# Performance work log

Hardware: AMD Instinct MI355X
Metric: run time of the kernel (lower is better)

The kernel has to match this reference:

```python
import jax, jax.numpy as jnp
import numpy as np

N0, N1, N2 = 360448, 22528, 2048
E0, E1 = 337920, 20480
D = 256


def setup_inputs() -> dict:
    key = jax.random.key(0)
    ks = jax.random.split(key, 12)
    s = 1.0 / np.sqrt(D)
    return {
        "x": jax.random.normal(ks[0], (N0, D), dtype=jnp.float32),
        "src0": jax.random.randint(ks[1], (E0,), 0, N0, dtype=jnp.int32),
        "dst0": jax.random.randint(ks[2], (E0,), 0, N1, dtype=jnp.int32),
        "src1": jax.random.randint(ks[3], (E1,), 0, N1, dtype=jnp.int32),
        "dst1": jax.random.randint(ks[4], (E1,), 0, N2, dtype=jnp.int32),
        "Wl0": jax.random.normal(ks[5], (D, D), dtype=jnp.float32) * s,
        "bl0": jnp.zeros((D,), dtype=jnp.float32),
        "Wr0": jax.random.normal(ks[6], (D, D), dtype=jnp.float32) * s,
        "Wl1": jax.random.normal(ks[7], (D, D), dtype=jnp.float32) * s,
        "bl1": jnp.zeros((D,), dtype=jnp.float32),
        "Wr1": jax.random.normal(ks[8], (D, D), dtype=jnp.float32) * s,
    }


def _sage_conv(x_src, x_tgt, src, dst, n_tgt, Wl, bl, Wr):
    # mean aggregation of source neighbor features per target node
    summed = jax.ops.segment_sum(x_src[src], dst, num_segments=n_tgt)
    cnt = jax.ops.segment_sum(jnp.ones((src.shape[0],), x_src.dtype), dst,
                              num_segments=n_tgt)
    agg = summed / jnp.maximum(cnt, 1.0)[:, None]
    # PyG SAGEConv: lin_l(agg) + lin_r(x_target); lin_r has no bias
    return agg @ Wl.T + bl + x_tgt @ Wr.T


def reference(x, src0, dst0, src1, dst1, Wl0, bl0, Wr0, Wl1, bl1, Wr1):
    # layer 0: [N0, D] -> [N1, D]
    h = _sage_conv(x, x[:N1], src0, dst0, N1, Wl0, bl0, Wr0)
    h = jax.nn.relu(h)  # dropout is identity in eval mode
    # layer 1: [N1, D] -> [N2, D]
    out = _sage_conv(h, h[:N2], src1, dst1, N2, Wl1, bl1, Wr1)
    return out
```

## Files before the change

### kernel.cpp

```cpp
#include <hip/hip_runtime.h>
#include <hip/hip_bf16.h>

#define N1C 22528
#define N2C 2048

typedef __attribute__((ext_vector_type(8))) short bf16x8;
typedef __attribute__((ext_vector_type(4))) float f32x4;

__device__ __forceinline__ short f2bf(float f) {
    union { float f; unsigned u; } x; x.f = f;
    unsigned r = x.u + 0x7fff + ((x.u >> 16) & 1);
    return (short)(r >> 16);
}
__device__ __forceinline__ float bf2f(unsigned short u) {
    union { unsigned u; float f; } x; x.u = ((unsigned)u) << 16;
    return x.f;
}

__global__ void prep_kernel(const float* __restrict__ Wl0, const float* __restrict__ Wr0,
                            const float* __restrict__ Wl1, const float* __restrict__ Wr1,
                            short* __restrict__ Wcat0, short* __restrict__ Wcat1,
                            int* __restrict__ hist0, int* __restrict__ hist1) {
    const int stride = gridDim.x * blockDim.x;
    const int tid0 = blockIdx.x * blockDim.x + threadIdx.x;
    for (int i = tid0; i < 2 * 256 * 512; i += stride) {
        int layer = i >> 17;
        int r = i & ((1 << 17) - 1);
        int j = r >> 9, k = r & 511;
        const float* Wl = layer ? Wl1 : Wl0;
        const float* Wr = layer ? Wr1 : Wr0;
        float v = (k < 256) ? Wl[j * 256 + k] : Wr[j * 256 + (k - 256)];
        (layer ? Wcat1 : Wcat0)[r] = f2bf(v);
    }
    for (int i = tid0; i < N1C + N2C; i += stride) {
        if (i < N1C) hist0[i] = 0; else hist1[i - N1C] = 0;
    }
}

__global__ void hist_both_kernel(const int* __restrict__ dst0, int E0,
                                 const int* __restrict__ dst1, int E1,
                                 int* __restrict__ hist0, int* __restrict__ hist1) {
    const int stride = gridDim.x * blockDim.x;
    for (int i = blockIdx.x * blockDim.x + threadIdx.x; i < E0 + E1; i += stride) {
        if (i < E0) atomicAdd(&hist0[dst0[i]], 1);
        else        atomicAdd(&hist1[dst1[i - E0]], 1);
    }
}

__global__ __launch_bounds__(1024)
void scan_both_kernel(const int* __restrict__ hist0, int* __restrict__ rowptr0,
                      int* __restrict__ cursor0,
                      const int* __restrict__ hist1, int* __restrict__ rowptr1,
                      int* __restrict__ cursor1) {
    __shared__ int sums[1024];
    const int N = (blockIdx.x == 0) ? N1C : N2C;
    const int* hist   = (blockIdx.x == 0) ? hist0 : hist1;
    int* rowptr       = (blockIdx.x == 0) ? rowptr0 : rowptr1;
    int* cursor       = (blockIdx.x == 0) ? cursor0 : cursor1;
    const int tid = threadIdx.x;
    const int per = (N + 1023) >> 10;
    const int start = tid * per;
    const int end = min(start + per, N);
    int s = 0;
    for (int i = start; i < end; ++i) s += hist[i];
    sums[tid] = s;
    __syncthreads();
    for (int d = 1; d < 1024; d <<= 1) {
        int t = (tid >= d) ? sums[tid - d] : 0;
        __syncthreads();
        sums[tid] += t;
        __syncthreads();
    }
    int off = sums[tid] - s;
    for (int i = start; i < end; ++i) {
        rowptr[i] = off;
        cursor[i] = off;
        off += hist[i];
    }
    if (tid == 1023) rowptr[N] = off;
}

__global__ void fill_both_kernel(const int* __restrict__ src0, const int* __restrict__ dst0, int E0,
                                 const int* __restrict__ src1, const int* __restrict__ dst1, int E1,
                                 int* __restrict__ cursor0, int* __restrict__ eidx0,
                                 int* __restrict__ cursor1, int* __restrict__ eidx1) {
    const int stride = gridDim.x * blockDim.x;
    for (int i = blockIdx.x * blockDim.x + threadIdx.x; i < E0 + E1; i += stride) {
        if (i < E0) {
            int p = atomicAdd(&cursor0[dst0[i]], 1);
            eidx0[p] = src0[i];
        } else {
            int p = atomicAdd(&cursor1[dst1[i - E0]], 1);
            eidx1[p] = src1[i - E0];
        }
    }
}

template <bool SRC_F32>
__global__ __launch_bounds__(256)
void gather_mean_kernel(const void* __restrict__ Xv, const int* __restrict__ rowptr,
                        const int* __restrict__ eidx, short* __restrict__ Acat, int N) {
    const int wv = (blockIdx.x * 256 + threadIdx.x) >> 6;
    const int lane = threadIdx.x & 63;
    if (wv >= N) return;
    const int beg = rowptr[wv];
    const int end = rowptr[wv + 1];
    float a0 = 0.f, a1 = 0.f, a2 = 0.f, a3 = 0.f;
    int j = beg;
    if (SRC_F32) {
        const float* X = (const float*)Xv;
        for (; j + 1 < end; j += 2) {
            int s0 = eidx[j], s1 = eidx[j + 1];
            float4 v0 = *(const float4*)(X + (size_t)s0 * 256 + lane * 4);
            float4 v1 = *(const float4*)(X + (size_t)s1 * 256 + lane * 4);
            a0 += v0.x + v1.x; a1 += v0.y + v1.y;
            a2 += v0.z + v1.z; a3 += v0.w + v1.w;
        }
        if (j < end) {
            float4 v0 = *(const float4*)(X + (size_t)eidx[j] * 256 + lane * 4);
            a0 += v0.x; a1 += v0.y; a2 += v0.z; a3 += v0.w;
        }
    } else {
        const ushort* X = (const ushort*)Xv;
        for (; j + 1 < end; j += 2) {
            int s0 = eidx[j], s1 = eidx[j + 1];
            ushort4 v0 = *(const ushort4*)(X + (size_t)s0 * 256 + lane * 4);
            ushort4 v1 = *(const ushort4*)(X + (size_t)s1 * 256 + lane * 4);
            a0 += bf2f(v0.x) + bf2f(v1.x); a1 += bf2f(v0.y) + bf2f(v1.y);
            a2 += bf2f(v0.z) + bf2f(v1.z); a3 += bf2f(v0.w) + bf2f(v1.w);
        }
        if (j < end) {
            ushort4 v0 = *(const ushort4*)(X + (size_t)eidx[j] * 256 + lane * 4);
            a0 += bf2f(v0.x); a1 += bf2f(v0.y); a2 += bf2f(v0.z); a3 += bf2f(v0.w);
        }
    }
    const float sc = 1.0f / fmaxf((float)(end - beg), 1.0f);
    short4 o;
    o.x = f2bf(a0 * sc); o.y = f2bf(a1 * sc);
    o.z = f2bf(a2 * sc); o.w = f2bf(a3 * sc);
    *(short4*)(Acat + (size_t)wv * 512 + lane * 4) = o;
}

__global__ void xcast_kernel(const float* __restrict__ x, short* __restrict__ Acat0) {
    const int stride = gridDim.x * blockDim.x;
    const int total = N1C * 64;
    for (int u = blockIdx.x * blockDim.x + threadIdx.x; u < total; u += stride) {
        int row = u >> 6;
        int c = (u & 63) * 4;
        float4 v = *(const float4*)(x + (size_t)row * 256 + c);
        short4 o;
        o.x = f2bf(v.x); o.y = f2bf(v.y); o.z = f2bf(v.z); o.w = f2bf(v.w);
        *(short4*)(Acat0 + (size_t)row * 512 + 256 + c) = o;
    }
}

template <bool RELU, bool OUT_BF16>
__global__ __launch_bounds__(256)
void mfma_gemm_kernel(const short* __restrict__ A, const short* __restrict__ W,
                      const float* __restrict__ bias, void* __restrict__ out,
                      short* __restrict__ out2, int M) {
    const int tid = threadIdx.x;
    const int wave = tid >> 6;
    const int lane = tid & 63;
    const int r0 = blockIdx.x * 64 + wave * 16;
    const int j0 = blockIdx.y * 64;
    const int lrow = lane & 15;
    const int lk = (lane >> 4) * 8;

    const short* arow = A + (size_t)(r0 + lrow) * 512 + lk;
    const short* wbase = W + (size_t)(j0 + lrow) * 512 + lk;

    f32x4 acc[4] = {f32x4{0,0,0,0}, f32x4{0,0,0,0}, f32x4{0,0,0,0}, f32x4{0,0,0,0}};
#pragma unroll
    for (int ks = 0; ks < 16; ++ks) {
        bf16x8 a = *(const bf16x8*)(arow + ks * 32);
#pragma unroll
        for (int c = 0; c < 4; ++c) {
            bf16x8 b = *(const bf16x8*)(wbase + (size_t)c * 16 * 512 + ks * 32);
            acc[c] = __builtin_amdgcn_mfma_f32_16x16x32_bf16(a, b, acc[c], 0, 0, 0);
        }
    }

    const int orow = (lane >> 4) * 4;
#pragma unroll
    for (int c = 0; c < 4; ++c) {
        const int col = j0 + c * 16 + lrow;
        const float bv = bias[col];
#pragma unroll
        for (int i = 0; i < 4; ++i) {
            const int row = r0 + orow + i;
            float v = acc[c][i] + bv;
            if (RELU) v = fmaxf(v, 0.0f);
            if (OUT_BF16) {
                short hv = f2bf(v);
                ((short*)out)[(size_t)row * 256 + col] = hv;
                if (out2 != nullptr && row < N2C)
                    out2[(size_t)row * 512 + 256 + col] = hv;
            } else {
                ((float*)out)[(size_t)row * 256 + col] = v;
            }
        }
    }
}

extern "C" void kernel_launch(void* const* d_in, const int* in_sizes, int n_in,
                              void* d_out, int out_size, void* d_ws, size_t ws_size,
                              hipStream_t stream) {
    const float* x    = (const float*)d_in[0];
    const int*   src0 = (const int*)d_in[1];
    const int*   dst0 = (const int*)d_in[2];
    const int*   src1 = (const int*)d_in[3];
    const int*   dst1 = (const int*)d_in[4];
    const float* Wl0  = (const float*)d_in[5];
    const float* bl0  = (const float*)d_in[6];
    const float* Wr0  = (const float*)d_in[7];
    const float* Wl1  = (const float*)d_in[8];
    const float* bl1  = (const float*)d_in[9];
    const float* Wr1  = (const float*)d_in[10];

    const int E0 = in_sizes[1];
    const int E1 = in_sizes[3];

    char* p = (char*)d_ws;
    short* Acat0 = (short*)p;            p += (size_t)N1C * 512 * 2;
    short* h     = (short*)p;            p += (size_t)N1C * 256 * 2;
    short* Acat1 = (short*)p;            p += (size_t)N2C * 512 * 2;
    short* Wcat0 = (short*)p;            p += 256 * 512 * 2;
    short* Wcat1 = (short*)p;            p += 256 * 512 * 2;
    int* hist0   = (int*)p;              p += (size_t)N1C * 4;
    int* cursor0 = (int*)p;              p += (size_t)N1C * 4;
    int* rowptr0 = (int*)p;              p += (size_t)(N1C + 4) * 4;
    int* hist1   = (int*)p;              p += (size_t)N2C * 4;
    int* cursor1 = (int*)p;              p += (size_t)N2C * 4;
    int* rowptr1 = (int*)p;              p += (size_t)(N2C + 4) * 4;
    int* eidx0   = (int*)p;              p += (size_t)E0 * 4;
    int* eidx1   = (int*)p;              p += (size_t)E1 * 4;

    prep_kernel<<<512, 256, 0, stream>>>(Wl0, Wr0, Wl1, Wr1, Wcat0, Wcat1, hist0, hist1);
    hist_both_kernel<<<512, 256, 0, stream>>>(dst0, E0, dst1, E1, hist0, hist1);
    scan_both_kernel<<<2, 1024, 0, stream>>>(hist0, rowptr0, cursor0, hist1, rowptr1, cursor1);
    fill_both_kernel<<<512, 256, 0, stream>>>(src0, dst0, E0, src1, dst1, E1,
                                              cursor0, eidx0, cursor1, eidx1);
    xcast_kernel<<<1024, 256, 0, stream>>>(x, Acat0);
    gather_mean_kernel<true><<<(N1C * 64 + 255) / 256, 256, 0, stream>>>(
        x, rowptr0, eidx0, Acat0, N1C);
    mfma_gemm_kernel<true, true><<<dim3(N1C / 64, 4), 256, 0, stream>>>(
        Acat0, Wcat0, bl0, h, Acat1, N1C);
    gather_mean_kernel<false><<<(N2C * 64 + 255) / 256, 256, 0, stream>>>(
        h, rowptr1, eidx1, Acat1, N2C);
    mfma_gemm_kernel<false, false><<<dim3(N2C / 64, 4), 256, 0, stream>>>(
        Acat1, Wcat1, bl1, (float*)d_out, nullptr, N2C);
}
```

Before: 224.2 us.

## Fuse x cast into layer-0 gather, unroll gather by 4, widen layer-0 GEMM tile

Folds the separate kernel that casts x to bf16 into the layer-0 gather kernel, so each wave writes both halves of its Acat0 row and one launch plus a pass over x go away. The layer-0 gather loop is unrolled to four neighbours with two accumulators to keep more loads in flight. The layer-0 GEMM now has each block cover all 256 output columns (CT=16), so each A tile is loaded once rather than four times. This raises register pressure (64 accumulator floats per lane) and cuts the layer-0 grid to 352 blocks, which may hurt occupancy.

```diff
diff --git a/kernel.cpp b/kernel.cpp
--- a/kernel.cpp
+++ b/kernel.cpp
@@ -96,10 +96,51 @@
     }
 }
 
-template <bool SRC_F32>
 __global__ __launch_bounds__(256)
-void gather_mean_kernel(const void* __restrict__ Xv, const int* __restrict__ rowptr,
-                        const int* __restrict__ eidx, short* __restrict__ Acat, int N) {
+void gather0_kernel(const float* __restrict__ x, const int* __restrict__ rowptr,
+                    const int* __restrict__ eidx, short* __restrict__ Acat0) {
+    const int wv = (blockIdx.x * 256 + threadIdx.x) >> 6;
+    const int lane = threadIdx.x & 63;
+    if (wv >= N1C) return;
+
+    const float4 xr = *(const float4*)(x + (size_t)wv * 256 + lane * 4);
+
+    const int beg = rowptr[wv];
+    const int end = rowptr[wv + 1];
+    float4 acc = {0.f, 0.f, 0.f, 0.f};
+    float4 acc2 = {0.f, 0.f, 0.f, 0.f};
+    int j = beg;
+    for (; j + 3 < end; j += 4) {
+        const int e0 = eidx[j], e1 = eidx[j + 1], e2 = eidx[j + 2], e3 = eidx[j + 3];
+        const float4 v0 = *(const float4*)(x + (size_t)e0 * 256 + lane * 4);
+        const float4 v1 = *(const float4*)(x + (size_t)e1 * 256 + lane * 4);
+        const float4 v2 = *(const float4*)(x + (size_t)e2 * 256 + lane * 4);
+        const float4 v3 = *(const float4*)(x + (size_t)e3 * 256 + lane * 4);
+        acc.x += v0.x + v1.x;  acc.y += v0.y + v1.y;
+        acc.z += v0.z + v1.z;  acc.w += v0.w + v1.w;
+        acc2.x += v2.x + v3.x; acc2.y += v2.y + v3.y;
+        acc2.z += v2.z + v3.z; acc2.w += v2.w + v3.w;
+    }
+    for (; j < end; ++j) {
+        const float4 v0 = *(const float4*)(x + (size_t)eidx[j] * 256 + lane * 4);
+        acc.x += v0.x; acc.y += v0.y; acc.z += v0.z; acc.w += v0.w;
+    }
+    acc.x += acc2.x; acc.y += acc2.y; acc.z += acc2.z; acc.w += acc2.w;
+
+    const float sc = 1.0f / fmaxf((float)(end - beg), 1.0f);
+    short4 o;
+    o.x = f2bf(acc.x * sc); o.y = f2bf(acc.y * sc);
+    o.z = f2bf(acc.z * sc); o.w = f2bf(acc.w * sc);
+    *(short4*)(Acat0 + (size_t)wv * 512 + lane * 4) = o;
+
+    short4 xo;
+    xo.x = f2bf(xr.x); xo.y = f2bf(xr.y); xo.z = f2bf(xr.z); xo.w = f2bf(xr.w);
+    *(short4*)(Acat0 + (size_t)wv * 512 + 256 + lane * 4) = xo;
+}
+
+__global__ __launch_bounds__(256)
+void gather1_kernel(const ushort* __restrict__ X, const int* __restrict__ rowptr,
+                    const int* __restrict__ eidx, short* __restrict__ Acat, int N) {
     const int wv = (blockIdx.x * 256 + threadIdx.x) >> 6;
     const int lane = threadIdx.x & 63;
     if (wv >= N) return;
@@ -107,32 +148,16 @@
     const int end = rowptr[wv + 1];
     float a0 = 0.f, a1 = 0.f, a2 = 0.f, a3 = 0.f;
     int j = beg;
-    if (SRC_F32) {
-        const float* X = (const float*)Xv;
-        for (; j + 1 < end; j += 2) {
-            int s0 = eidx[j], s1 = eidx[j + 1];
-            float4 v0 = *(const float4*)(X + (size_t)s0 * 256 + lane * 4);
-            float4 v1 = *(const float4*)(X + (size_t)s1 * 256 + lane * 4);
-            a0 += v0.x + v1.x; a1 += v0.y + v1.y;
-            a2 += v0.z + v1.z; a3 += v0.w + v1.w;
-        }
-        if (j < end) {
-            float4 v0 = *(const float4*)(X + (size_t)eidx[j] * 256 + lane * 4);
-            a0 += v0.x; a1 += v0.y; a2 += v0.z; a3 += v0.w;
-        }
-    } else {
-        const ushort* X = (const ushort*)Xv;
-        for (; j + 1 < end; j += 2) {
-            int s0 = eidx[j], s1 = eidx[j + 1];
-            ushort4 v0 = *(const ushort4*)(X + (size_t)s0 * 256 + lane * 4);
-            ushort4 v1 = *(const ushort4*)(X + (size_t)s1 * 256 + lane * 4);
-            a0 += bf2f(v0.x) + bf2f(v1.x); a1 += bf2f(v0.y) + bf2f(v1.y);
-            a2 += bf2f(v0.z) + bf2f(v1.z); a3 += bf2f(v0.w) + bf2f(v1.w);
-        }
-        if (j < end) {
-            ushort4 v0 = *(const ushort4*)(X + (size_t)eidx[j] * 256 + lane * 4);
-            a0 += bf2f(v0.x); a1 += bf2f(v0.y); a2 += bf2f(v0.z); a3 += bf2f(v0.w);
-        }
+    for (; j + 1 < end; j += 2) {
+        int s0 = eidx[j], s1 = eidx[j + 1];
+        ushort4 v0 = *(const ushort4*)(X + (size_t)s0 * 256 + lane * 4);
+        ushort4 v1 = *(const ushort4*)(X + (size_t)s1 * 256 + lane * 4);
+        a0 += bf2f(v0.x) + bf2f(v1.x); a1 += bf2f(v0.y) + bf2f(v1.y);
+        a2 += bf2f(v0.z) + bf2f(v1.z); a3 += bf2f(v0.w) + bf2f(v1.w);
+    }
+    if (j < end) {
+        ushort4 v0 = *(const ushort4*)(X + (size_t)eidx[j] * 256 + lane * 4);
+        a0 += bf2f(v0.x); a1 += bf2f(v0.y); a2 += bf2f(v0.z); a3 += bf2f(v0.w);
     }
     const float sc = 1.0f / fmaxf((float)(end - beg), 1.0f);
     short4 o;
@@ -141,20 +166,7 @@
     *(short4*)(Acat + (size_t)wv * 512 + lane * 4) = o;
 }
 
-__global__ void xcast_kernel(const float* __restrict__ x, short* __restrict__ Acat0) {
-    const int stride = gridDim.x * blockDim.x;
-    const int total = N1C * 64;
-    for (int u = blockIdx.x * blockDim.x + threadIdx.x; u < total; u += stride) {
-        int row = u >> 6;
-        int c = (u & 63) * 4;
-        float4 v = *(const float4*)(x + (size_t)row * 256 + c);
-        short4 o;
-        o.x = f2bf(v.x); o.y = f2bf(v.y); o.z = f2bf(v.z); o.w = f2bf(v.w);
-        *(short4*)(Acat0 + (size_t)row * 512 + 256 + c) = o;
-    }
-}
-
-template <bool RELU, bool OUT_BF16>
+template <int CT, bool RELU, bool OUT_BF16>
 __global__ __launch_bounds__(256)
 void mfma_gemm_kernel(const short* __restrict__ A, const short* __restrict__ W,
                       const float* __restrict__ bias, void* __restrict__ out,
@@ -163,19 +175,18 @@
     const int wave = tid >> 6;
     const int lane = tid & 63;
     const int r0 = blockIdx.x * 64 + wave * 16;
-    const int j0 = blockIdx.y * 64;
+    const int j0 = blockIdx.y * (CT * 16);
     const int lrow = lane & 15;
     const int lk = (lane >> 4) * 8;
 
     const short* arow = A + (size_t)(r0 + lrow) * 512 + lk;
     const short* wbase = W + (size_t)(j0 + lrow) * 512 + lk;
 
-    f32x4 acc[4] = {f32x4{0,0,0,0}, f32x4{0,0,0,0}, f32x4{0,0,0,0}, f32x4{0,0,0,0}};
-#pragma unroll
+    f32x4 acc[CT] = {};
     for (int ks = 0; ks < 16; ++ks) {
         bf16x8 a = *(const bf16x8*)(arow + ks * 32);
 #pragma unroll
-        for (int c = 0; c < 4; ++c) {
+        for (int c = 0; c < CT; ++c) {
             bf16x8 b = *(const bf16x8*)(wbase + (size_t)c * 16 * 512 + ks * 32);
             acc[c] = __builtin_amdgcn_mfma_f32_16x16x32_bf16(a, b, acc[c], 0, 0, 0);
         }
@@ -183,7 +194,7 @@
 
     const int orow = (lane >> 4) * 4;
 #pragma unroll
-    for (int c = 0; c < 4; ++c) {
+    for (int c = 0; c < CT; ++c) {
         const int col = j0 + c * 16 + lrow;
         const float bv = bias[col];
 #pragma unroll
@@ -241,13 +252,11 @@
     scan_both_kernel<<<2, 1024, 0, stream>>>(hist0, rowptr0, cursor0, hist1, rowptr1, cursor1);
     fill_both_kernel<<<512, 256, 0, stream>>>(src0, dst0, E0, src1, dst1, E1,
                                               cursor0, eidx0, cursor1, eidx1);
-    xcast_kernel<<<1024, 256, 0, stream>>>(x, Acat0);
-    gather_mean_kernel<true><<<(N1C * 64 + 255) / 256, 256, 0, stream>>>(
-        x, rowptr0, eidx0, Acat0, N1C);
-    mfma_gemm_kernel<true, true><<<dim3(N1C / 64, 4), 256, 0, stream>>>(
+    gather0_kernel<<<(N1C * 64 + 255) / 256, 256, 0, stream>>>(x, rowptr0, eidx0, Acat0);
+    mfma_gemm_kernel<16, true, true><<<dim3(N1C / 64, 1), 256, 0, stream>>>(
         Acat0, Wcat0, bl0, h, Acat1, N1C);
-    gather_mean_kernel<false><<<(N2C * 64 + 255) / 256, 256, 0, stream>>>(
-        h, rowptr1, eidx1, Acat1, N2C);
-    mfma_gemm_kernel<false, false><<<dim3(N2C / 64, 4), 256, 0, stream>>>(
+    gather1_kernel<<<(N2C * 64 + 255) / 256, 256, 0, stream>>>(
+        (const ushort*)h, rowptr1, eidx1, Acat1, N2C);
+    mfma_gemm_kernel<4, false, false><<<dim3(N2C / 64, 4), 256, 0, stream>>>(
         Acat1, Wcat1, bl1, (float*)d_out, nullptr, N2C);
 }
```

New measurement: 231.7 us. 1.03x slower.
